# Kernel tuning notes

Measured on AMD Instinct MI355X. Metric: run time of the kernel, lower is better.

## Reference

```python
import jax, jax.numpy as jnp
import numpy as np

N = 100000      # nodes
E = 1600000     # edges (avg degree 16)
F_IN = 128      # num_features
H = 64          # hidden_dim
C = 7           # num_classes


def setup_inputs() -> dict:
    key = jax.random.key(0)
    ks = jax.random.split(key, 9)
    x = jax.random.normal(ks[0], (N, F_IN), dtype=jnp.float32)
    edge_index = jax.random.randint(ks[1], (2, E), 0, N, dtype=jnp.int32)
    s1 = 1.0 / np.sqrt(F_IN)
    s2 = 1.0 / np.sqrt(H)
    # SAGEConv1: lin_l applied to aggregated neighbors, lin_r to root
    W1l = jax.random.uniform(ks[2], (F_IN, H), jnp.float32, -s1, s1)
    W1r = jax.random.uniform(ks[3], (F_IN, H), jnp.float32, -s1, s1)
    b1 = jax.random.uniform(ks[4], (H,), jnp.float32, -s1, s1)
    # SAGEConv2
    W2l = jax.random.uniform(ks[5], (H, C), jnp.float32, -s2, s2)
    W2r = jax.random.uniform(ks[6], (H, C), jnp.float32, -s2, s2)
    b2 = jax.random.uniform(ks[7], (C,), jnp.float32, -s2, s2)
    return {"x": x, "edge_index": edge_index, "W1l": W1l, "W1r": W1r,
            "b1": b1, "W2l": W2l, "W2r": W2r, "b2": b2}


def _segment_mean(vals, idx, num_segments):
    # scatter-mean: sum messages per destination node, divide by in-degree
    sums = jax.ops.segment_sum(vals, idx, num_segments=num_segments)
    cnt = jax.ops.segment_sum(jnp.ones(idx.shape, vals.dtype), idx,
                              num_segments=num_segments)
    return sums / jnp.maximum(cnt, 1.0)[:, None]


def reference(x, edge_index, W1l, W1r, b1, W2l, W2r, b2):
    src, dst = edge_index[0], edge_index[1]
    # SAGEConv 1: mean of neighbor (src) features at each dst, plus root term
    agg1 = _segment_mean(x[src], dst, N)              # [N, F_IN]
    h = agg1 @ W1l + x @ W1r + b1                     # [N, H]
    h = jax.nn.relu(h)
    # dropout is inactive in eval mode (deterministic reference)
    # SAGEConv 2
    agg2 = _segment_mean(h[src], dst, N)              # [N, H]
    out = agg2 @ W2l + h @ W2r + b2                   # [N, C]
    return jax.nn.log_softmax(out, axis=1)
```

## Files before the change

kernel.cpp:

```cpp
#include <hip/hip_runtime.h>
#include <cstdint>
#include <cstddef>


#define CAP 64
#define BINSZ 128
#define CH 4096

typedef __attribute__((ext_vector_type(8))) short bf16x8v;
typedef __attribute__((ext_vector_type(4))) float f32x4v;

__device__ __forceinline__ float bf2f(unsigned short u) {
  return __uint_as_float(((unsigned int)u) << 16);
}
__device__ __forceinline__ unsigned short f2bf(float f) {
  unsigned int x = __float_as_uint(f);
  unsigned int r = (x + 0x7fffu + ((x >> 16) & 1u)) >> 16;
  return (unsigned short)r;
}

__global__ __launch_bounds__(256) void k_hist(const int* __restrict__ ei,
                                              int* __restrict__ hist,
                                              const float* __restrict__ W1l,
                                              const float* __restrict__ W1r,
                                              unsigned short* __restrict__ wswz,
                                              int E, int NB, int NCH) {
  const int t = threadIdx.x;
  if (blockIdx.x >= (unsigned)NCH) {
    int idx = (blockIdx.x - NCH) * 256 + t;
    int j = idx & 7;
    int lane = (idx >> 3) & 63;
    int c = (idx >> 9) & 7;
    int t4 = idx >> 12;
    int kk = t4 * 32 + (lane >> 4) * 8 + j;
    int nn = c * 16 + (lane & 15);
    float v = (nn < 64) ? W1l[kk * 64 + nn] : W1r[kk * 64 + (nn - 64)];
    wswz[idx] = f2bf(v);
    return;
  }
  __shared__ int lcnt[1024];
  const int c = blockIdx.x;
  for (int i = t; i < NB; i += 256) lcnt[i] = 0;
  __syncthreads();
  const int base = c * CH;
  const int end = min(base + CH, E);
  for (int e = base + t; e < end; e += 256) {
    int d = ei[E + e];
    atomicAdd(&lcnt[d >> 7], 1);
  }
  __syncthreads();
  for (int i = t; i < NB; i += 256) hist[(size_t)i * NCH + c] = lcnt[i];
}

__global__ __launch_bounds__(256) void k_scanA(int* __restrict__ hist,
                                               int* __restrict__ tot,
                                               int NB, int NCH) {
  const int lane = threadIdx.x & 63;
  const int bin = blockIdx.x * 4 + (threadIdx.x >> 6);
  if (bin >= NB) return;
  int* h = hist + (size_t)bin * NCH;
  int carry = 0;
  for (int base = 0; base < NCH; base += 64) {
    int i = base + lane;
    int v = (i < NCH) ? h[i] : 0;
    int incl = v;
    #pragma unroll
    for (int d = 1; d < 64; d <<= 1) {
      int t = __shfl_up(incl, d, 64);
      if (lane >= d) incl += t;
    }
    if (i < NCH) h[i] = carry + incl - v;
    carry += __shfl(incl, 63, 64);
  }
  if (lane == 0) tot[bin] = carry;
}

__global__ __launch_bounds__(64) void k_scanB(const int* __restrict__ tot,
                                              int* __restrict__ binbase, int NB) {
  const int lane = threadIdx.x;
  int carry = 0;
  for (int base = 0; base < NB; base += 64) {
    int i = base + lane;
    int v = (i < NB) ? tot[i] : 0;
    int incl = v;
    #pragma unroll
    for (int d = 1; d < 64; d <<= 1) {
      int t = __shfl_up(incl, d, 64);
      if (lane >= d) incl += t;
    }
    if (i < NB) binbase[i] = carry + incl - v;
    carry += __shfl(incl, 63, 64);
  }
  if (lane == 0) binbase[NB] = carry;
}

__global__ __launch_bounds__(256) void k_scat(const int* __restrict__ ei,
                                              const int* __restrict__ hist,
                                              const int* __restrict__ binbase,
                                              unsigned int* __restrict__ part,
                                              int E, int NB, int NCH) {
  __shared__ int lcur[1024];
  const int c = blockIdx.x, t = threadIdx.x;
  for (int i = t; i < NB; i += 256)
    lcur[i] = hist[(size_t)i * NCH + c] + binbase[i];
  __syncthreads();
  const int base = c * CH;
  const int end = min(base + CH, E);
  for (int e = base + t; e < end; e += 256) {
    int s = ei[e];
    int d = ei[E + e];
    int bin = d >> 7;
    int pos = atomicAdd(&lcur[bin], 1);
    part[pos] = (unsigned)s | ((unsigned)(d & 127) << 17);
  }
}

__global__ __launch_bounds__(256) void k_bucketB(const int* __restrict__ binbase,
                                                 const unsigned int* __restrict__ part,
                                                 int* __restrict__ cnt,
                                                 int* __restrict__ bucket) {
  __shared__ int lbkt[BINSZ * CAP];
  __shared__ int ldeg[BINSZ];
  const int b = blockIdx.x, t = threadIdx.x;
  if (t < BINSZ) ldeg[t] = 0;
  __syncthreads();
  const int e0 = binbase[b], e1 = binbase[b + 1];
  for (int i = e0 + t; i < e1; i += 256) {
    unsigned rec = part[i];
    int loc = rec >> 17;
    int p = atomicAdd(&ldeg[loc], 1);
    if (p < CAP) lbkt[loc * CAP + p] = (int)(rec & 0x1FFFFu);
  }
  __syncthreads();
  if (t < BINSZ) cnt[b * BINSZ + t] = ldeg[t];
  const int4* s4 = (const int4*)lbkt;
  int4* d4 = (int4*)(bucket + (size_t)b * BINSZ * CAP);
  #pragma unroll 2
  for (int i = t; i < BINSZ * CAP / 4; i += 256) d4[i] = s4[i];
}

__global__ __launch_bounds__(256) void k_gemm1(
    const float* __restrict__ x,
    const unsigned short* __restrict__ wswz,
    const float* __restrict__ b1,
    unsigned short* __restrict__ xl,
    unsigned short* __restrict__ hroot,
    int Nn) {
  __shared__ unsigned short Bsw[16384];
  const int t = threadIdx.x;
  {
    const uint4* src = (const uint4*)wswz;
    uint4* dst = (uint4*)Bsw;
    #pragma unroll
    for (int i = 0; i < 8; ++i) dst[t + i * 256] = src[t + i * 256];
  }
  __syncthreads();

  const int lane = t & 63;
  const int wid = t >> 6;
  const int quad = lane >> 4;
  const int m = lane & 15;
  const int rowA = blockIdx.x * 64 + wid * 16 + m;
  const float* xrow = x + (size_t)min(rowA, Nn - 1) * 128;

  f32x4v acc[8];
  #pragma unroll
  for (int c = 0; c < 8; ++c) acc[c] = (f32x4v){0.f, 0.f, 0.f, 0.f};

  #pragma unroll
  for (int t4 = 0; t4 < 4; ++t4) {
    const int koff = t4 * 32 + quad * 8;
    float4 a0 = *(const float4*)(xrow + koff);
    float4 a1 = *(const float4*)(xrow + koff + 4);
    bf16x8v af;
    af[0] = (short)f2bf(a0.x); af[1] = (short)f2bf(a0.y);
    af[2] = (short)f2bf(a0.z); af[3] = (short)f2bf(a0.w);
    af[4] = (short)f2bf(a1.x); af[5] = (short)f2bf(a1.y);
    af[6] = (short)f2bf(a1.z); af[7] = (short)f2bf(a1.w);
    #pragma unroll
    for (int c = 0; c < 8; ++c) {
      const bf16x8v bf_ = *(const bf16x8v*)&Bsw[(((t4 * 8 + c) * 64 + lane)) << 3];
      acc[c] = __builtin_amdgcn_mfma_f32_16x16x32_bf16(af, bf_, acc[c], 0, 0, 0);
    }
  }

  const int rbase = blockIdx.x * 64 + wid * 16 + quad * 4;
  #pragma unroll
  for (int c = 0; c < 8; ++c) {
    const int col = c * 16 + m;
    #pragma unroll
    for (int i = 0; i < 4; ++i) {
      const int r = rbase + i;
      if (r < Nn) {
        if (c < 4) xl[(size_t)r * 64 + col] = f2bf(acc[c][i]);
        else       hroot[(size_t)r * 64 + (col - 64)] = f2bf(acc[c][i] + b1[col - 64]);
      }
    }
  }
}

__global__ __launch_bounds__(256) void k_agg1(
    const int* __restrict__ cnt, const int* __restrict__ bucket,
    const unsigned int* __restrict__ xl32, const unsigned int* __restrict__ hroot32,
    unsigned int* __restrict__ hbuf32, int Nn) {
  const int lane = threadIdx.x & 63;
  const int q = lane & 15;
  const int g = lane >> 4;
  const int gw = blockIdx.x * (blockDim.x >> 6) + (threadIdx.x >> 6);
  const int nw = gridDim.x * (blockDim.x >> 6);
  for (int n = gw; n < Nn; n += nw) {
    int c = cnt[n];
    int m = c < CAP ? c : CAP;
    int sidx = (lane < m) ? bucket[(size_t)n * CAP + lane] : 0;
    if ((unsigned)sidx >= (unsigned)Nn) sidx = 0;
    uint2 hu = *(const uint2*)(hroot32 + (size_t)n * 32 + 2 * q);
    float a0 = 0.f, a1 = 0.f, a2 = 0.f, a3 = 0.f;
    int i = 0;
    for (; i + 16 <= m; i += 16) {
      int rA = __shfl(sidx, i + g, 64);
      int rB = __shfl(sidx, i + 4 + g, 64);
      int rC = __shfl(sidx, i + 8 + g, 64);
      int rD = __shfl(sidx, i + 12 + g, 64);
      uint2 uA = *(const uint2*)(xl32 + (size_t)rA * 32 + 2 * q);
      uint2 uB = *(const uint2*)(xl32 + (size_t)rB * 32 + 2 * q);
      uint2 uC = *(const uint2*)(xl32 + (size_t)rC * 32 + 2 * q);
      uint2 uD = *(const uint2*)(xl32 + (size_t)rD * 32 + 2 * q);
      a0 += (__uint_as_float(uA.x << 16) + __uint_as_float(uB.x << 16))
          + (__uint_as_float(uC.x << 16) + __uint_as_float(uD.x << 16));
      a1 += (__uint_as_float(uA.x & 0xFFFF0000u) + __uint_as_float(uB.x & 0xFFFF0000u))
          + (__uint_as_float(uC.x & 0xFFFF0000u) + __uint_as_float(uD.x & 0xFFFF0000u));
      a2 += (__uint_as_float(uA.y << 16) + __uint_as_float(uB.y << 16))
          + (__uint_as_float(uC.y << 16) + __uint_as_float(uD.y << 16));
      a3 += (__uint_as_float(uA.y & 0xFFFF0000u) + __uint_as_float(uB.y & 0xFFFF0000u))
          + (__uint_as_float(uC.y & 0xFFFF0000u) + __uint_as_float(uD.y & 0xFFFF0000u));
    }
    for (; i + 8 <= m; i += 8) {
      int rA = __shfl(sidx, i + g, 64);
      int rB = __shfl(sidx, i + 4 + g, 64);
      uint2 uA = *(const uint2*)(xl32 + (size_t)rA * 32 + 2 * q);
      uint2 uB = *(const uint2*)(xl32 + (size_t)rB * 32 + 2 * q);
      a0 += __uint_as_float(uA.x << 16) + __uint_as_float(uB.x << 16);
      a1 += __uint_as_float(uA.x & 0xFFFF0000u) + __uint_as_float(uB.x & 0xFFFF0000u);
      a2 += __uint_as_float(uA.y << 16) + __uint_as_float(uB.y << 16);
      a3 += __uint_as_float(uA.y & 0xFFFF0000u) + __uint_as_float(uB.y & 0xFFFF0000u);
    }
    for (; i < m; i += 4) {
      int e = i + g;
      int r = __shfl(sidx, e & 63, 64);
      uint2 u = *(const uint2*)(xl32 + (size_t)r * 32 + 2 * q);
      if (e < m) {
        a0 += __uint_as_float(u.x << 16);
        a1 += __uint_as_float(u.x & 0xFFFF0000u);
        a2 += __uint_as_float(u.y << 16);
        a3 += __uint_as_float(u.y & 0xFFFF0000u);
      }
    }
    a0 += __shfl_xor(a0, 16, 64); a0 += __shfl_xor(a0, 32, 64);
    a1 += __shfl_xor(a1, 16, 64); a1 += __shfl_xor(a1, 32, 64);
    a2 += __shfl_xor(a2, 16, 64); a2 += __shfl_xor(a2, 32, 64);
    a3 += __shfl_xor(a3, 16, 64); a3 += __shfl_xor(a3, 32, 64);
    if (g == 0) {
      float dd = c > 0 ? (float)c : 1.f;
      float h0 = fmaxf(a0 / dd + __uint_as_float(hu.x << 16), 0.f);
      float h1 = fmaxf(a1 / dd + __uint_as_float(hu.x & 0xFFFF0000u), 0.f);
      float h2 = fmaxf(a2 / dd + __uint_as_float(hu.y << 16), 0.f);
      float h3 = fmaxf(a3 / dd + __uint_as_float(hu.y & 0xFFFF0000u), 0.f);
      uint2 o;
      o.x = (unsigned)f2bf(h0) | ((unsigned)f2bf(h1) << 16);
      o.y = (unsigned)f2bf(h2) | ((unsigned)f2bf(h3) << 16);
      *(uint2*)(hbuf32 + (size_t)n * 32 + 2 * q) = o;
    }
  }
}

__global__ __launch_bounds__(128) void k_gemm2(
    const unsigned short* __restrict__ hbuf,
    const float* __restrict__ W2l, const float* __restrict__ W2r,
    const float* __restrict__ b2,
    float* __restrict__ hl, float* __restrict__ hr, int Nn) {
  __shared__ float tile[128 * 65];
  const int t = threadIdx.x;
  const int rowbase = blockIdx.x * 128;
  for (int idx = t; idx < 128 * 64; idx += 128) {
    int r = idx >> 6, k = idx & 63;
    int n = rowbase + r;
    tile[r * 65 + k] = (n < Nn) ? bf2f(hbuf[(size_t)n * 64 + k]) : 0.f;
  }
  __syncthreads();
  int n = rowbase + t;
  if (n >= Nn) return;
  float al[7] = {0, 0, 0, 0, 0, 0, 0};
  float ar[7] = {0, 0, 0, 0, 0, 0, 0};
  for (int k = 0; k < 64; ++k) {
    float hv = tile[t * 65 + k];
    #pragma unroll
    for (int c = 0; c < 7; ++c) {
      al[c] = fmaf(hv, W2l[k * 7 + c], al[c]);
      ar[c] = fmaf(hv, W2r[k * 7 + c], ar[c]);
    }
  }
  #pragma unroll
  for (int c = 0; c < 7; ++c) {
    hl[(size_t)n * 8 + c] = al[c];
    hr[(size_t)n * 8 + c] = ar[c] + b2[c];
  }
  hl[(size_t)n * 8 + 7] = 0.f;
  hr[(size_t)n * 8 + 7] = 0.f;
}

__global__ __launch_bounds__(256) void k_out(
    const int* __restrict__ cnt, const int* __restrict__ bucket,
    const float* __restrict__ hl, const float* __restrict__ hr,
    float* __restrict__ out, int Nn) {
  const int lane = threadIdx.x & 63;
  const int c = lane & 7;
  const int sub = lane >> 3;
  const int gw = blockIdx.x * (blockDim.x >> 6) + (threadIdx.x >> 6);
  const int n = gw * 8 + sub;
  if (n >= Nn) return;
  int cn = cnt[n];
  int m = cn < CAP ? cn : CAP;
  const bool act = (c < 7);
  float acc = 0.f;
  for (int e0 = 0; e0 < m; e0 += 8) {
    int bv = (e0 + c < m) ? bucket[(size_t)n * CAP + e0 + c] : 0;
    #pragma unroll
    for (int cc = 0; cc < 8; ++cc) {
      if (e0 + cc < m) {
        int s = __shfl(bv, (lane & 56) + cc, 64);
        if ((unsigned)s >= (unsigned)Nn) s = 0;
        if (act) acc += hl[(size_t)s * 8 + c];
      }
    }
  }
  float dd = cn > 0 ? (float)cn : 1.f;
  float v = act ? (acc / dd + hr[(size_t)n * 8 + c]) : -INFINITY;
  float mx = v;
  mx = fmaxf(mx, __shfl_xor(mx, 1, 8));
  mx = fmaxf(mx, __shfl_xor(mx, 2, 8));
  mx = fmaxf(mx, __shfl_xor(mx, 4, 8));
  float ex = act ? expf(v - mx) : 0.f;
  float s2 = ex;
  s2 += __shfl_xor(s2, 1, 8);
  s2 += __shfl_xor(s2, 2, 8);
  s2 += __shfl_xor(s2, 4, 8);
  float res = v - mx - logf(s2);
  if (act) out[(size_t)n * 7 + c] = res;
}

static inline size_t alignup(size_t v) { return (v + 255) & ~(size_t)255; }

extern "C" void kernel_launch(void* const* d_in, const int* in_sizes, int n_in,
                              void* d_out, int out_size, void* d_ws, size_t ws_size,
                              hipStream_t stream) {
  const int N = in_sizes[0] / 128;
  const int E = in_sizes[1] / 2;
  const int NB = (N + BINSZ - 1) / BINSZ;
  const int Np = NB * BINSZ;
  const int NCH = (E + CH - 1) / CH;

  const float* x   = (const float*)d_in[0];
  const int*   ei  = (const int*)d_in[1];
  const float* W1l = (const float*)d_in[2];
  const float* W1r = (const float*)d_in[3];
  const float* b1  = (const float*)d_in[4];
  const float* W2l = (const float*)d_in[5];
  const float* W2r = (const float*)d_in[6];
  const float* b2  = (const float*)d_in[7];
  float* out = (float*)d_out;

  char* p = (char*)d_ws;
  int* hist    = (int*)p;            p += alignup((size_t)NB * NCH * 4);
  int* tot     = (int*)p;            p += alignup((size_t)NB * 4);
  int* binbase = (int*)p;            p += alignup((size_t)(NB + 1) * 4);
  unsigned int* part = (unsigned int*)p; p += alignup((size_t)E * 4);
  int* cnt    = (int*)p;             p += alignup((size_t)Np * 4);
  int* bucket = (int*)p;             p += alignup((size_t)Np * CAP * 4);
  unsigned short* wswz = (unsigned short*)p; p += alignup((size_t)16384 * 2);
  unsigned short* xl    = (unsigned short*)p; p += alignup((size_t)N * 64 * 2);
  unsigned short* hroot = (unsigned short*)p; p += alignup((size_t)N * 64 * 2);
  unsigned short* hbuf  = (unsigned short*)p; p += alignup((size_t)N * 64 * 2);
  float* hl  = (float*)p;            p += alignup((size_t)N * 8 * 4);
  float* hr  = (float*)p;            p += alignup((size_t)N * 8 * 4);

  dim3 b256(256);
  k_hist<<<dim3(NCH + 64), b256, 0, stream>>>(ei, hist, W1l, W1r, wswz, E, NB, NCH);
  k_scanA<<<dim3((NB + 3) / 4), b256, 0, stream>>>(hist, tot, NB, NCH);
  k_scanB<<<dim3(1), dim3(64), 0, stream>>>(tot, binbase, NB);
  k_scat<<<dim3(NCH), b256, 0, stream>>>(ei, hist, binbase, part, E, NB, NCH);
  k_bucketB<<<dim3(NB), b256, 0, stream>>>(binbase, part, cnt, bucket);
  k_gemm1<<<dim3((N + 63) / 64), b256, 0, stream>>>(x, wswz, b1, xl, hroot, N);
  k_agg1<<<dim3(2048), b256, 0, stream>>>(cnt, bucket,
      (const unsigned int*)xl, (const unsigned int*)hroot, (unsigned int*)hbuf, N);
  k_gemm2<<<dim3((N + 127) / 128), dim3(128), 0, stream>>>(hbuf, W2l, W2r, b2, hl, hr, N);
  const int waves_out = (N + 7) / 8;
  k_out<<<dim3((waves_out + 3) / 4), b256, 0, stream>>>(cnt, bucket, hl, hr, out, N);
}
```

Baseline: 253.6 us.

## Merge histogram scan with first GEMM and prefetch next node in aggregation

The per-bin histogram scan and the first dense GEMM now run in one launch, with block ranges selecting the role, so the small latency-bound scan overlaps the GEMM and one launch goes away. The aggregation loop is also software-pipelined: it loads the next node's count, neighbour indices and root row before processing the current node. This hides gather latency at the cost of extra registers. The merged GEMM blocks also get the shared-memory footprint in every block, which may reduce scan occupancy.

```diff
diff --git a/kernel.cpp b/kernel.cpp
--- a/kernel.cpp
+++ b/kernel.cpp
@@ -52,102 +52,35 @@
   for (int i = t; i < NB; i += 256) hist[(size_t)i * NCH + c] = lcnt[i];
 }
 
-__global__ __launch_bounds__(256) void k_scanA(int* __restrict__ hist,
-                                               int* __restrict__ tot,
-                                               int NB, int NCH) {
-  const int lane = threadIdx.x & 63;
-  const int bin = blockIdx.x * 4 + (threadIdx.x >> 6);
-  if (bin >= NB) return;
-  int* h = hist + (size_t)bin * NCH;
-  int carry = 0;
-  for (int base = 0; base < NCH; base += 64) {
-    int i = base + lane;
-    int v = (i < NCH) ? h[i] : 0;
-    int incl = v;
-    #pragma unroll
-    for (int d = 1; d < 64; d <<= 1) {
-      int t = __shfl_up(incl, d, 64);
-      if (lane >= d) incl += t;
-    }
-    if (i < NCH) h[i] = carry + incl - v;
-    carry += __shfl(incl, 63, 64);
-  }
-  if (lane == 0) tot[bin] = carry;
-}
-
-__global__ __launch_bounds__(64) void k_scanB(const int* __restrict__ tot,
-                                              int* __restrict__ binbase, int NB) {
-  const int lane = threadIdx.x;
-  int carry = 0;
-  for (int base = 0; base < NB; base += 64) {
-    int i = base + lane;
-    int v = (i < NB) ? tot[i] : 0;
-    int incl = v;
-    #pragma unroll
-    for (int d = 1; d < 64; d <<= 1) {
-      int t = __shfl_up(incl, d, 64);
-      if (lane >= d) incl += t;
-    }
-    if (i < NB) binbase[i] = carry + incl - v;
-    carry += __shfl(incl, 63, 64);
-  }
-  if (lane == 0) binbase[NB] = carry;
-}
-
-__global__ __launch_bounds__(256) void k_scat(const int* __restrict__ ei,
-                                              const int* __restrict__ hist,
-                                              const int* __restrict__ binbase,
-                                              unsigned int* __restrict__ part,
-                                              int E, int NB, int NCH) {
-  __shared__ int lcur[1024];
-  const int c = blockIdx.x, t = threadIdx.x;
-  for (int i = t; i < NB; i += 256)
-    lcur[i] = hist[(size_t)i * NCH + c] + binbase[i];
-  __syncthreads();
-  const int base = c * CH;
-  const int end = min(base + CH, E);
-  for (int e = base + t; e < end; e += 256) {
-    int s = ei[e];
-    int d = ei[E + e];
-    int bin = d >> 7;
-    int pos = atomicAdd(&lcur[bin], 1);
-    part[pos] = (unsigned)s | ((unsigned)(d & 127) << 17);
-  }
-}
-
-__global__ __launch_bounds__(256) void k_bucketB(const int* __restrict__ binbase,
-                                                 const unsigned int* __restrict__ part,
-                                                 int* __restrict__ cnt,
-                                                 int* __restrict__ bucket) {
-  __shared__ int lbkt[BINSZ * CAP];
-  __shared__ int ldeg[BINSZ];
-  const int b = blockIdx.x, t = threadIdx.x;
-  if (t < BINSZ) ldeg[t] = 0;
-  __syncthreads();
-  const int e0 = binbase[b], e1 = binbase[b + 1];
-  for (int i = e0 + t; i < e1; i += 256) {
-    unsigned rec = part[i];
-    int loc = rec >> 17;
-    int p = atomicAdd(&ldeg[loc], 1);
-    if (p < CAP) lbkt[loc * CAP + p] = (int)(rec & 0x1FFFFu);
-  }
-  __syncthreads();
-  if (t < BINSZ) cnt[b * BINSZ + t] = ldeg[t];
-  const int4* s4 = (const int4*)lbkt;
-  int4* d4 = (int4*)(bucket + (size_t)b * BINSZ * CAP);
-  #pragma unroll 2
-  for (int i = t; i < BINSZ * CAP / 4; i += 256) d4[i] = s4[i];
-}
-
-__global__ __launch_bounds__(256) void k_gemm1(
-    const float* __restrict__ x,
-    const unsigned short* __restrict__ wswz,
-    const float* __restrict__ b1,
-    unsigned short* __restrict__ xl,
-    unsigned short* __restrict__ hroot,
-    int Nn) {
+__global__ __launch_bounds__(256) void k_scan_gemm(
+    int* __restrict__ hist, int* __restrict__ tot, int NB, int NCH, int nScan,
+    const float* __restrict__ x, const unsigned short* __restrict__ wswz,
+    const float* __restrict__ b1, unsigned short* __restrict__ xl,
+    unsigned short* __restrict__ hroot, int Nn) {
+  if (blockIdx.x < (unsigned)nScan) {
+    const int lane = threadIdx.x & 63;
+    const int bin = blockIdx.x * 4 + (threadIdx.x >> 6);
+    if (bin >= NB) return;
+    int* h = hist + (size_t)bin * NCH;
+    int carry = 0;
+    for (int base = 0; base < NCH; base += 64) {
+      int i = base + lane;
+      int v = (i < NCH) ? h[i] : 0;
+      int incl = v;
+      #pragma unroll
+      for (int d = 1; d < 64; d <<= 1) {
+        int t = __shfl_up(incl, d, 64);
+        if (lane >= d) incl += t;
+      }
+      if (i < NCH) h[i] = carry + incl - v;
+      carry += __shfl(incl, 63, 64);
+    }
+    if (lane == 0) tot[bin] = carry;
+    return;
+  }
   __shared__ unsigned short Bsw[16384];
   const int t = threadIdx.x;
+  const int bid = blockIdx.x - nScan;
   {
     const uint4* src = (const uint4*)wswz;
     uint4* dst = (uint4*)Bsw;
@@ -160,7 +93,7 @@
   const int wid = t >> 6;
   const int quad = lane >> 4;
   const int m = lane & 15;
-  const int rowA = blockIdx.x * 64 + wid * 16 + m;
+  const int rowA = bid * 64 + wid * 16 + m;
   const float* xrow = x + (size_t)min(rowA, Nn - 1) * 128;
 
   f32x4v acc[8];
@@ -184,7 +117,7 @@
     }
   }
 
-  const int rbase = blockIdx.x * 64 + wid * 16 + quad * 4;
+  const int rbase = bid * 64 + wid * 16 + quad * 4;
   #pragma unroll
   for (int c = 0; c < 8; ++c) {
     const int col = c * 16 + m;
@@ -197,6 +130,70 @@
       }
     }
   }
+}
+
+__global__ __launch_bounds__(64) void k_scanB(const int* __restrict__ tot,
+                                              int* __restrict__ binbase, int NB) {
+  const int lane = threadIdx.x;
+  int carry = 0;
+  for (int base = 0; base < NB; base += 64) {
+    int i = base + lane;
+    int v = (i < NB) ? tot[i] : 0;
+    int incl = v;
+    #pragma unroll
+    for (int d = 1; d < 64; d <<= 1) {
+      int t = __shfl_up(incl, d, 64);
+      if (lane >= d) incl += t;
+    }
+    if (i < NB) binbase[i] = carry + incl - v;
+    carry += __shfl(incl, 63, 64);
+  }
+  if (lane == 0) binbase[NB] = carry;
+}
+
+__global__ __launch_bounds__(256) void k_scat(const int* __restrict__ ei,
+                                              const int* __restrict__ hist,
+                                              const int* __restrict__ binbase,
+                                              unsigned int* __restrict__ part,
+                                              int E, int NB, int NCH) {
+  __shared__ int lcur[1024];
+  const int c = blockIdx.x, t = threadIdx.x;
+  for (int i = t; i < NB; i += 256)
+    lcur[i] = hist[(size_t)i * NCH + c] + binbase[i];
+  __syncthreads();
+  const int base = c * CH;
+  const int end = min(base + CH, E);
+  for (int e = base + t; e < end; e += 256) {
+    int s = ei[e];
+    int d = ei[E + e];
+    int bin = d >> 7;
+    int pos = atomicAdd(&lcur[bin], 1);
+    part[pos] = (unsigned)s | ((unsigned)(d & 127) << 17);
+  }
+}
+
+__global__ __launch_bounds__(256) void k_bucketB(const int* __restrict__ binbase,
+                                                 const unsigned int* __restrict__ part,
+                                                 int* __restrict__ cnt,
+                                                 int* __restrict__ bucket) {
+  __shared__ int lbkt[BINSZ * CAP];
+  __shared__ int ldeg[BINSZ];
+  const int b = blockIdx.x, t = threadIdx.x;
+  if (t < BINSZ) ldeg[t] = 0;
+  __syncthreads();
+  const int e0 = binbase[b], e1 = binbase[b + 1];
+  for (int i = e0 + t; i < e1; i += 256) {
+    unsigned rec = part[i];
+    int loc = rec >> 17;
+    int p = atomicAdd(&ldeg[loc], 1);
+    if (p < CAP) lbkt[loc * CAP + p] = (int)(rec & 0x1FFFFu);
+  }
+  __syncthreads();
+  if (t < BINSZ) cnt[b * BINSZ + t] = ldeg[t];
+  const int4* s4 = (const int4*)lbkt;
+  int4* d4 = (int4*)(bucket + (size_t)b * BINSZ * CAP);
+  #pragma unroll 2
+  for (int i = t; i < BINSZ * CAP / 4; i += 256) d4[i] = s4[i];
 }
 
 __global__ __launch_bounds__(256) void k_agg1(
@@ -206,14 +203,25 @@
   const int lane = threadIdx.x & 63;
   const int q = lane & 15;
   const int g = lane >> 4;
-  const int gw = blockIdx.x * (blockDim.x >> 6) + (threadIdx.x >> 6);
   const int nw = gridDim.x * (blockDim.x >> 6);
-  for (int n = gw; n < Nn; n += nw) {
-    int c = cnt[n];
-    int m = c < CAP ? c : CAP;
-    int sidx = (lane < m) ? bucket[(size_t)n * CAP + lane] : 0;
-    if ((unsigned)sidx >= (unsigned)Nn) sidx = 0;
-    uint2 hu = *(const uint2*)(hroot32 + (size_t)n * 32 + 2 * q);
+  int n = blockIdx.x * (blockDim.x >> 6) + (threadIdx.x >> 6);
+  if (n >= Nn) return;
+
+  int c  = cnt[n];
+  int c1 = cnt[min(n + nw, Nn - 1)];
+  int m = c < CAP ? c : CAP;
+  int sidx = (lane < m) ? bucket[(size_t)n * CAP + lane] : 0;
+  if ((unsigned)sidx >= (unsigned)Nn) sidx = 0;
+  uint2 hu = *(const uint2*)(hroot32 + (size_t)n * 32 + 2 * q);
+
+  while (true) {
+    const int n1 = n + nw;
+    const int n1c = min(n1, Nn - 1);
+    const int m1 = c1 < CAP ? c1 : CAP;
+    int sidx1 = (lane < m1) ? bucket[(size_t)n1c * CAP + lane] : 0;
+    uint2 hu1 = *(const uint2*)(hroot32 + (size_t)n1c * 32 + 2 * q);
+    int c2 = cnt[min(n1 + nw, Nn - 1)];
+
     float a0 = 0.f, a1 = 0.f, a2 = 0.f, a3 = 0.f;
     int i = 0;
     for (; i + 16 <= m; i += 16) {
@@ -270,6 +278,10 @@
       o.y = (unsigned)f2bf(h2) | ((unsigned)f2bf(h3) << 16);
       *(uint2*)(hbuf32 + (size_t)n * 32 + 2 * q) = o;
     }
+    if (n1 >= Nn) break;
+    n = n1; c = c1; c1 = c2; m = m1;
+    sidx = ((unsigned)sidx1 >= (unsigned)Nn) ? 0 : sidx1;
+    hu = hu1;
   }
 }
 
@@ -358,6 +370,7 @@
   const int NB = (N + BINSZ - 1) / BINSZ;
   const int Np = NB * BINSZ;
   const int NCH = (E + CH - 1) / CH;
+  const int nScan = (NB + 3) / 4;
 
   const float* x   = (const float*)d_in[0];
   const int*   ei  = (const int*)d_in[1];
@@ -385,11 +398,11 @@
 
   dim3 b256(256);
   k_hist<<<dim3(NCH + 64), b256, 0, stream>>>(ei, hist, W1l, W1r, wswz, E, NB, NCH);
-  k_scanA<<<dim3((NB + 3) / 4), b256, 0, stream>>>(hist, tot, NB, NCH);
+  k_scan_gemm<<<dim3(nScan + (N + 63) / 64), b256, 0, stream>>>(
+      hist, tot, NB, NCH, nScan, x, wswz, b1, xl, hroot, N);
   k_scanB<<<dim3(1), dim3(64), 0, stream>>>(tot, binbase, NB);
   k_scat<<<dim3(NCH), b256, 0, stream>>>(ei, hist, binbase, part, E, NB, NCH);
   k_bucketB<<<dim3(NB), b256, 0, stream>>>(binbase, part, cnt, bucket);
-  k_gemm1<<<dim3((N + 63) / 64), b256, 0, stream>>>(x, wswz, b1, xl, hroot, N);
   k_agg1<<<dim3(2048), b256, 0, stream>>>(cnt, bucket,
       (const unsigned int*)xl, (const unsigned int*)hroot, (unsigned int*)hbuf, N);
   k_gemm2<<<dim3((N + 127) / 128), dim3(128), 0, stream>>>(hbuf, W2l, W2r, b2, hl, hr, N);
```

Result: faster. 241.9 us (-4.6%).

## Replace binned counting-sort CSR build with global atomic bucketing fused into GEMM1

Applied to the files above, without the earlier changes.

Drops the histogram, two scan kernels, partition scatter and per-bin bucketing. The adjacency buckets are now built directly with a global atomicAdd on each destination's degree counter, and that work runs in the same launch as the first GEMM using disjoint block ranges. A small prep kernel swizzles the weights and zeroes the counters. This cuts four kernel launches and the intermediate passes over the edge list, but bucket writes become scattered across a large array and neighbor order inside each bucket is now nondeterministic.

```diff
diff --git a/kernel.cpp b/kernel.cpp
--- a/kernel.cpp
+++ b/kernel.cpp
@@ -4,7 +4,6 @@
 
 
 #define CAP 64
-#define BINSZ 128
 #define CH 4096
 
 typedef __attribute__((ext_vector_type(8))) short bf16x8v;
@@ -19,15 +18,13 @@
   return (unsigned short)r;
 }
 
-__global__ __launch_bounds__(256) void k_hist(const int* __restrict__ ei,
-                                              int* __restrict__ hist,
-                                              const float* __restrict__ W1l,
+__global__ __launch_bounds__(256) void k_prep(const float* __restrict__ W1l,
                                               const float* __restrict__ W1r,
                                               unsigned short* __restrict__ wswz,
-                                              int E, int NB, int NCH) {
+                                              int* __restrict__ cnt, int Nn) {
   const int t = threadIdx.x;
-  if (blockIdx.x >= (unsigned)NCH) {
-    int idx = (blockIdx.x - NCH) * 256 + t;
+  if (blockIdx.x < 64) {
+    int idx = blockIdx.x * 256 + t;
     int j = idx & 7;
     int lane = (idx >> 3) & 63;
     int c = (idx >> 9) & 7;
@@ -38,116 +35,30 @@
     wswz[idx] = f2bf(v);
     return;
   }
-  __shared__ int lcnt[1024];
-  const int c = blockIdx.x;
-  for (int i = t; i < NB; i += 256) lcnt[i] = 0;
-  __syncthreads();
-  const int base = c * CH;
-  const int end = min(base + CH, E);
-  for (int e = base + t; e < end; e += 256) {
-    int d = ei[E + e];
-    atomicAdd(&lcnt[d >> 7], 1);
-  }
-  __syncthreads();
-  for (int i = t; i < NB; i += 256) hist[(size_t)i * NCH + c] = lcnt[i];
-}
-
-__global__ __launch_bounds__(256) void k_scanA(int* __restrict__ hist,
-                                               int* __restrict__ tot,
-                                               int NB, int NCH) {
-  const int lane = threadIdx.x & 63;
-  const int bin = blockIdx.x * 4 + (threadIdx.x >> 6);
-  if (bin >= NB) return;
-  int* h = hist + (size_t)bin * NCH;
-  int carry = 0;
-  for (int base = 0; base < NCH; base += 64) {
-    int i = base + lane;
-    int v = (i < NCH) ? h[i] : 0;
-    int incl = v;
-    #pragma unroll
-    for (int d = 1; d < 64; d <<= 1) {
-      int t = __shfl_up(incl, d, 64);
-      if (lane >= d) incl += t;
-    }
-    if (i < NCH) h[i] = carry + incl - v;
-    carry += __shfl(incl, 63, 64);
-  }
-  if (lane == 0) tot[bin] = carry;
-}
-
-__global__ __launch_bounds__(64) void k_scanB(const int* __restrict__ tot,
-                                              int* __restrict__ binbase, int NB) {
-  const int lane = threadIdx.x;
-  int carry = 0;
-  for (int base = 0; base < NB; base += 64) {
-    int i = base + lane;
-    int v = (i < NB) ? tot[i] : 0;
-    int incl = v;
-    #pragma unroll
-    for (int d = 1; d < 64; d <<= 1) {
-      int t = __shfl_up(incl, d, 64);
-      if (lane >= d) incl += t;
-    }
-    if (i < NB) binbase[i] = carry + incl - v;
-    carry += __shfl(incl, 63, 64);
-  }
-  if (lane == 0) binbase[NB] = carry;
-}
-
-__global__ __launch_bounds__(256) void k_scat(const int* __restrict__ ei,
-                                              const int* __restrict__ hist,
-                                              const int* __restrict__ binbase,
-                                              unsigned int* __restrict__ part,
-                                              int E, int NB, int NCH) {
-  __shared__ int lcur[1024];
-  const int c = blockIdx.x, t = threadIdx.x;
-  for (int i = t; i < NB; i += 256)
-    lcur[i] = hist[(size_t)i * NCH + c] + binbase[i];
-  __syncthreads();
-  const int base = c * CH;
-  const int end = min(base + CH, E);
-  for (int e = base + t; e < end; e += 256) {
-    int s = ei[e];
-    int d = ei[E + e];
-    int bin = d >> 7;
-    int pos = atomicAdd(&lcur[bin], 1);
-    part[pos] = (unsigned)s | ((unsigned)(d & 127) << 17);
-  }
-}
-
-__global__ __launch_bounds__(256) void k_bucketB(const int* __restrict__ binbase,
-                                                 const unsigned int* __restrict__ part,
-                                                 int* __restrict__ cnt,
-                                                 int* __restrict__ bucket) {
-  __shared__ int lbkt[BINSZ * CAP];
-  __shared__ int ldeg[BINSZ];
-  const int b = blockIdx.x, t = threadIdx.x;
-  if (t < BINSZ) ldeg[t] = 0;
-  __syncthreads();
-  const int e0 = binbase[b], e1 = binbase[b + 1];
-  for (int i = e0 + t; i < e1; i += 256) {
-    unsigned rec = part[i];
-    int loc = rec >> 17;
-    int p = atomicAdd(&ldeg[loc], 1);
-    if (p < CAP) lbkt[loc * CAP + p] = (int)(rec & 0x1FFFFu);
-  }
-  __syncthreads();
-  if (t < BINSZ) cnt[b * BINSZ + t] = ldeg[t];
-  const int4* s4 = (const int4*)lbkt;
-  int4* d4 = (int4*)(bucket + (size_t)b * BINSZ * CAP);
-  #pragma unroll 2
-  for (int i = t; i < BINSZ * CAP / 4; i += 256) d4[i] = s4[i];
-}
-
-__global__ __launch_bounds__(256) void k_gemm1(
-    const float* __restrict__ x,
-    const unsigned short* __restrict__ wswz,
-    const float* __restrict__ b1,
-    unsigned short* __restrict__ xl,
-    unsigned short* __restrict__ hroot,
-    int Nn) {
+  int i4 = (blockIdx.x - 64) * 256 + t;
+  int n4 = (Nn + 3) >> 2;
+  if (i4 < n4) *(int4*)(cnt + i4 * 4) = make_int4(0, 0, 0, 0);
+}
+
+__global__ __launch_bounds__(256) void k_build_gemm(
+    const int* __restrict__ ei, int* __restrict__ cnt, int* __restrict__ bucket,
+    const float* __restrict__ x, const unsigned short* __restrict__ wswz,
+    const float* __restrict__ b1, unsigned short* __restrict__ xl,
+    unsigned short* __restrict__ hroot, int E, int NCH, int Nn) {
+  const int t = threadIdx.x;
+  if (blockIdx.x < (unsigned)NCH) {
+    const int base = blockIdx.x * CH;
+    const int end = min(base + CH, E);
+    for (int e = base + t; e < end; e += 256) {
+      int s = ei[e];
+      int d = ei[E + e];
+      int p = atomicAdd(&cnt[d], 1);
+      if (p < CAP) bucket[(size_t)d * CAP + p] = s;
+    }
+    return;
+  }
   __shared__ unsigned short Bsw[16384];
-  const int t = threadIdx.x;
+  const int bid = blockIdx.x - NCH;
   {
     const uint4* src = (const uint4*)wswz;
     uint4* dst = (uint4*)Bsw;
@@ -160,7 +71,7 @@
   const int wid = t >> 6;
   const int quad = lane >> 4;
   const int m = lane & 15;
-  const int rowA = blockIdx.x * 64 + wid * 16 + m;
+  const int rowA = bid * 64 + wid * 16 + m;
   const float* xrow = x + (size_t)min(rowA, Nn - 1) * 128;
 
   f32x4v acc[8];
@@ -184,7 +95,7 @@
     }
   }
 
-  const int rbase = blockIdx.x * 64 + wid * 16 + quad * 4;
+  const int rbase = bid * 64 + wid * 16 + quad * 4;
   #pragma unroll
   for (int c = 0; c < 8; ++c) {
     const int col = c * 16 + m;
@@ -355,8 +266,6 @@
                               hipStream_t stream) {
   const int N = in_sizes[0] / 128;
   const int E = in_sizes[1] / 2;
-  const int NB = (N + BINSZ - 1) / BINSZ;
-  const int Np = NB * BINSZ;
   const int NCH = (E + CH - 1) / CH;
 
   const float* x   = (const float*)d_in[0];
@@ -370,12 +279,8 @@
   float* out = (float*)d_out;
 
   char* p = (char*)d_ws;
-  int* hist    = (int*)p;            p += alignup((size_t)NB * NCH * 4);
-  int* tot     = (int*)p;            p += alignup((size_t)NB * 4);
-  int* binbase = (int*)p;            p += alignup((size_t)(NB + 1) * 4);
-  unsigned int* part = (unsigned int*)p; p += alignup((size_t)E * 4);
-  int* cnt    = (int*)p;             p += alignup((size_t)Np * 4);
-  int* bucket = (int*)p;             p += alignup((size_t)Np * CAP * 4);
+  int* cnt    = (int*)p;             p += alignup(((size_t)N + 4) * 4);
+  int* bucket = (int*)p;             p += alignup((size_t)N * CAP * 4);
   unsigned short* wswz = (unsigned short*)p; p += alignup((size_t)16384 * 2);
   unsigned short* xl    = (unsigned short*)p; p += alignup((size_t)N * 64 * 2);
   unsigned short* hroot = (unsigned short*)p; p += alignup((size_t)N * 64 * 2);
@@ -384,12 +289,10 @@
   float* hr  = (float*)p;            p += alignup((size_t)N * 8 * 4);
 
   dim3 b256(256);
-  k_hist<<<dim3(NCH + 64), b256, 0, stream>>>(ei, hist, W1l, W1r, wswz, E, NB, NCH);
-  k_scanA<<<dim3((NB + 3) / 4), b256, 0, stream>>>(hist, tot, NB, NCH);
-  k_scanB<<<dim3(1), dim3(64), 0, stream>>>(tot, binbase, NB);
-  k_scat<<<dim3(NCH), b256, 0, stream>>>(ei, hist, binbase, part, E, NB, NCH);
-  k_bucketB<<<dim3(NB), b256, 0, stream>>>(binbase, part, cnt, bucket);
-  k_gemm1<<<dim3((N + 63) / 64), b256, 0, stream>>>(x, wswz, b1, xl, hroot, N);
+  const int nZero = (((N + 3) / 4) + 255) / 256;
+  k_prep<<<dim3(64 + nZero), b256, 0, stream>>>(W1l, W1r, wswz, cnt, N);
+  k_build_gemm<<<dim3(NCH + (N + 63) / 64), b256, 0, stream>>>(
+      ei, cnt, bucket, x, wswz, b1, xl, hroot, E, NCH, N);
   k_agg1<<<dim3(2048), b256, 0, stream>>>(cnt, bucket,
       (const unsigned int*)xl, (const unsigned int*)hroot, (unsigned int*)hbuf, N);
   k_gemm2<<<dim3((N + 127) / 128), dim3(128), 0, stream>>>(hbuf, W2l, W2r, b2, hl, hr, N);
```

After: 307.8 us. 1.21x slower.
